# Kernel optimization log

Measured on AMD Instinct MI355X. Metric: run time of the kernel, lower is better.

## Reference

```python
import jax, jax.numpy as jnp
import numpy as np

N = 50000        # number of amino_acid nodes
E = 250000       # edges per relation
HID = 64         # resid_hidden_dim (per-head out dim)
H = 4            # num_heads
L = 2            # resid_num_layers
IN_DIM = 256     # input_dim (fc_dim output)
SCALE = 1.0 / np.sqrt(HID)
EPS_BN = 1e-5


def setup_inputs() -> dict:
    key = jax.random.key(0)
    ks = jax.random.split(key, 12)
    inp = {"x": jax.random.normal(ks[0], (N, HID), jnp.float32)}
    for i, nm in enumerate(("seq", "knn", "dis")):
        inp[f"src_{nm}"] = jax.random.randint(ks[1 + 2 * i], (E,), 0, N, dtype=jnp.int32)
        inp[f"dst_{nm}"] = jax.random.randint(ks[2 + 2 * i], (E,), 0, N, dtype=jnp.int32)
    s = 0.05
    inp["Wsrc"] = jax.random.normal(ks[7], (L, 3, HID, H * HID), jnp.float32) * s
    inp["Wdst"] = jax.random.normal(ks[8], (L, 3, HID, H * HID), jnp.float32) * s
    inp["Wfc"] = jax.random.normal(ks[9], (L, HID, HID), jnp.float32) * s
    inp["bfc"] = jnp.zeros((L, HID), jnp.float32)
    inp["gamma"] = jnp.ones((L, HID), jnp.float32)
    inp["beta"] = jnp.zeros((L, HID), jnp.float32)
    inp["Wdim"] = jax.random.normal(ks[10], (HID, IN_DIM), jnp.float32) * s
    inp["bdim"] = jnp.zeros((IN_DIM,), jnp.float32)
    return inp


def _gat_dot(x, Wsrc, Wdst, src, dst):
    # GATDotConv: q/k projections, scaled dot-product attention per edge,
    # edge-softmax over incoming edges per destination, sum aggregation.
    fs = (x @ Wsrc).reshape(N, H, HID)   # key/value (source) features
    fd = (x @ Wdst).reshape(N, H, HID)   # query (destination) features
    e = jnp.einsum("ehd,ehd->eh", fs[src], fd[dst]) * SCALE   # [E, H]
    m = jax.ops.segment_max(e, dst, num_segments=N)           # [N, H]
    m = jnp.where(jnp.isfinite(m), m, 0.0)                    # zero-in-degree safe
    p = jnp.exp(e - m[dst])
    denom = jax.ops.segment_sum(p, dst, num_segments=N)       # [N, H]
    alpha = p / jnp.maximum(denom[dst], 1e-9)                 # [E, H]
    return jax.ops.segment_sum(fs[src] * alpha[:, :, None], dst, num_segments=N)  # [N, H, HID]


def _batchnorm(x, gamma, beta):
    mu = jnp.mean(x, axis=0)
    var = jnp.var(x, axis=0)
    return gamma * (x - mu) * jax.lax.rsqrt(var + EPS_BN) + beta


def reference(x, src_seq, dst_seq, src_knn, dst_knn, src_dis, dst_dis,
              Wsrc, Wdst, Wfc, bfc, gamma, beta, Wdim, bdim):
    edges = ((src_seq, dst_seq), (src_knn, dst_knn), (src_dis, dst_dis))
    h = x
    for l in range(L):
        # HeteroGraphConv with aggregate='sum' over the three relations
        agg = jnp.zeros((N, H, HID), h.dtype)
        for r in range(3):
            agg = agg + _gat_dot(h, Wsrc[l, r], Wdst[l, r], edges[r][0], edges[r][1])
        h = jnp.mean(agg, axis=1)                       # mean over heads -> [N, HID]
        h = _batchnorm(jax.nn.relu(h @ Wfc[l] + bfc[l]), gamma[l], beta[l])
        # dropout omitted (identity in eval / deterministic reference)
    return h @ Wdim + bdim                              # [N, IN_DIM]
```

## Files before the change

kernel.cpp:

```cpp
#include <hip/hip_runtime.h>
#include <math.h>

#define N_NODES 50000
#define E_EDGES 250000
#define HID 64
#define HD 256
#define L_LAYERS 2
#define IN_DIM_ 256
#define ATT_SCALE 0.125f
#define LOG2E 1.44269504f
#define EPS_BN 1e-5f
#define NCHUNK 49
#define GX 782

#define PACK_REL (6 * 512 * 64)
#define PACK_FC  (2 * 64 * 64)
#define PACK_DIM (256 * 64)
#define HIST_B   2930
#define PACK_B   864
#define CVT_B    3125
#define PROJ_B   (GX * 8 * 3)

#define TS 72

typedef __attribute__((ext_vector_type(8))) short bf16x8;
typedef __attribute__((ext_vector_type(4))) float f32x4;

static __device__ __forceinline__ unsigned short f2bf(float f) {
    unsigned u = __float_as_uint(f);
    unsigned r = (u + 0x7fff + ((u >> 16) & 1)) >> 16;
    return (unsigned short)r;
}
static __device__ __forceinline__ float bf2f(unsigned u) {
    return __uint_as_float(u << 16);
}

static __device__ __forceinline__ float rowsum16(float x) {
    int t;
    t = __builtin_amdgcn_update_dpp(0, __float_as_int(x), 0xB1, 0xf, 0xf, true);
    x += __int_as_float(t);
    t = __builtin_amdgcn_update_dpp(0, __float_as_int(x), 0x4E, 0xf, 0xf, true);
    x += __int_as_float(t);
    t = __builtin_amdgcn_update_dpp(0, __float_as_int(x), 0x141, 0xf, 0xf, true);
    x += __int_as_float(t);
    t = __builtin_amdgcn_update_dpp(0, __float_as_int(x), 0x140, 0xf, 0xf, true);
    x += __int_as_float(t);
    return x;
}


__global__ __launch_bounds__(256) void scan_partial(const int* __restrict__ count,
                                                    int* __restrict__ bsum) {
    int b = blockIdx.x;
    int r = b / NCHUNK, ch = b - r * NCHUNK;
    int tid = threadIdx.x;
    int i0 = ch * 1024 + tid * 4;
    int s = 0;
    if (i0 + 3 < N_NODES) {
        int4 v = *(const int4*)(count + r * N_NODES + i0);
        s = v.x + v.y + v.z + v.w;
    } else {
        for (int j = 0; j < 4; ++j)
            if (i0 + j < N_NODES) s += count[r * N_NODES + i0 + j];
    }
    for (int o = 1; o < 64; o <<= 1) s += __shfl_xor(s, o, 64);
    __shared__ int wsum[4];
    if ((tid & 63) == 0) wsum[tid >> 6] = s;
    __syncthreads();
    if (tid == 0) bsum[b] = wsum[0] + wsum[1] + wsum[2] + wsum[3];
}

__global__ __launch_bounds__(256) void scan_mid(const int* __restrict__ bsum,
                                                int* __restrict__ bpre) {
    __shared__ int A[256], B[256];
    int tid = threadIdx.x;
    int v = (tid < 3 * NCHUNK) ? bsum[tid] : 0;
    int segStart = (tid / NCHUNK) * NCHUNK;
    A[tid] = v;
    __syncthreads();
    int* s = A; int* d = B;
    for (int o = 1; o < 256; o <<= 1) {
        int x = s[tid];
        if (tid - o >= segStart) x += s[tid - o];
        d[tid] = x;
        __syncthreads();
        int* t = s; s = d; d = t;
    }
    if (tid < 3 * NCHUNK) bpre[tid] = s[tid] - v;
}

__global__ __launch_bounds__(256) void scan_final(const int* __restrict__ count,
                                                  const int* __restrict__ bpre,
                                                  int* __restrict__ row_off,
                                                  int* __restrict__ cursor) {
    int b = blockIdx.x;
    int r = b / NCHUNK, ch = b - r * NCHUNK;
    int tid = threadIdx.x;
    int i0 = ch * 1024 + tid * 4;
    int v[4] = {0, 0, 0, 0};
    if (i0 + 3 < N_NODES) {
        int4 t = *(const int4*)(count + r * N_NODES + i0);
        v[0] = t.x; v[1] = t.y; v[2] = t.z; v[3] = t.w;
    } else {
        for (int j = 0; j < 4; ++j)
            if (i0 + j < N_NODES) v[j] = count[r * N_NODES + i0 + j];
    }
    int tsum = v[0] + v[1] + v[2] + v[3];
    __shared__ int A[256], B[256];
    A[tid] = tsum;
    __syncthreads();
    int* s = A; int* d = B;
    for (int o = 1; o < 256; o <<= 1) {
        int x = s[tid];
        if (tid >= o) x += s[tid - o];
        d[tid] = x;
        __syncthreads();
        int* t = s; s = d; d = t;
    }
    int run = bpre[b] + s[tid] - tsum;
    int* ro = row_off + r * (N_NODES + 1);
    int* cu = cursor + r * N_NODES;
    for (int j = 0; j < 4; ++j) {
        int idx = i0 + j;
        if (idx < N_NODES) { ro[idx] = run; cu[idx] = run; run += v[j]; }
    }
    if (ch == NCHUNK - 1 && tid == 255) ro[N_NODES] = E_EDGES;
}


__global__ __launch_bounds__(256) void u1_kernel(
        const int* __restrict__ d0, const int* __restrict__ d1, const int* __restrict__ d2,
        int* __restrict__ count,
        const float* __restrict__ Wsrc, const float* __restrict__ Wdst,
        const float* __restrict__ Wfc, const float* __restrict__ Wdim,
        unsigned short* __restrict__ WtRel, unsigned short* __restrict__ WtFc,
        unsigned short* __restrict__ WtDim,
        const float* __restrict__ x, unsigned short* __restrict__ xb) {
    int b = blockIdx.x;
    if (b < HIST_B) {
        int i = b * 256 + threadIdx.x;
        if (i < 3 * E_EDGES) {
            int r = i / E_EDGES;
            int e = i - r * E_EDGES;
            const int* dst = (r == 0) ? d0 : ((r == 1) ? d1 : d2);
            atomicAdd(&count[r * N_NODES + dst[e]], 1);
        }
    } else if (b < HIST_B + PACK_B) {
        int i = (b - HIST_B) * 256 + threadIdx.x;
        if (i < PACK_REL) {
            int k = i & 63;
            int n = (i >> 6) & 511;
            int lr = i >> 15;
            const float* srcm = (n < 256) ? Wsrc : Wdst;
            WtRel[i] = f2bf(srcm[((size_t)lr * 64 + k) * 256 + (n & 255)]);
        } else if (i < PACK_REL + PACK_FC) {
            int j = i - PACK_REL;
            int l = j >> 12, rem = j & 4095;
            int k = rem & 63, n = rem >> 6;
            WtFc[j] = f2bf(Wfc[(size_t)l * 4096 + k * 64 + n]);
        } else if (i < PACK_REL + PACK_FC + PACK_DIM) {
            int j = i - PACK_REL - PACK_FC;
            int k = j & 63, n = j >> 6;
            WtDim[j] = f2bf(Wdim[(size_t)k * 256 + n]);
        }
    } else {
        int i = ((b - HIST_B - PACK_B) * 256 + threadIdx.x) * 4;
        if (i < N_NODES * HID) {
            float4 v = *(const float4*)(x + i);
            uint2 o;
            o.x = (unsigned)f2bf(v.x) | ((unsigned)f2bf(v.y) << 16);
            o.y = (unsigned)f2bf(v.z) | ((unsigned)f2bf(v.w) << 16);
            *(uint2*)(xb + i) = o;
        }
    }
}


static __device__ __forceinline__ void proj_body(int bx, int by,
        const unsigned short* __restrict__ hB, const unsigned short* __restrict__ Wt,
        unsigned short* __restrict__ out, int M, unsigned short* tile) {
    int tid = threadIdx.x;
    int wave = tid >> 6, lane = tid & 63;
    int q = lane >> 4, li = lane & 15;
    int nodeLoc = (wave >> 1) * 32;
    int featLoc = (wave & 1) * 32;
    int nodeBase = bx * 64 + nodeLoc;
    int featBase = by * 64 + featLoc;

    const unsigned short* aptr[2];
    const unsigned short* bptr[2];
    #pragma unroll
    for (int t = 0; t < 2; ++t) {
        aptr[t] = Wt + (size_t)(featBase + t * 16 + li) * 64 + q * 8;
        int node = nodeBase + t * 16 + li; if (node >= M) node = M - 1;
        bptr[t] = hB + (size_t)node * 64 + q * 8;
    }
    f32x4 acc[2][2];
    #pragma unroll
    for (int a = 0; a < 2; ++a)
        #pragma unroll
        for (int bq = 0; bq < 2; ++bq)
            #pragma unroll
            for (int i = 0; i < 4; ++i) acc[a][bq][i] = 0.f;

    #pragma unroll
    for (int s = 0; s < 2; ++s) {
        bf16x8 a[2], b[2];
        #pragma unroll
        for (int t = 0; t < 2; ++t) {
            a[t] = *(const bf16x8*)(aptr[t] + s * 32);
            b[t] = *(const bf16x8*)(bptr[t] + s * 32);
        }
        #pragma unroll
        for (int ft = 0; ft < 2; ++ft)
            #pragma unroll
            for (int nt = 0; nt < 2; ++nt)
                acc[ft][nt] = __builtin_amdgcn_mfma_f32_16x16x32_bf16(a[ft], b[nt], acc[ft][nt], 0, 0, 0);
    }
    #pragma unroll
    for (int ft = 0; ft < 2; ++ft) {
        int fl = featLoc + ft * 16 + q * 4;
        #pragma unroll
        for (int nt = 0; nt < 2; ++nt) {
            int nl = nodeLoc + nt * 16 + li;
            unsigned lo = (unsigned)f2bf(acc[ft][nt][0]) | ((unsigned)f2bf(acc[ft][nt][1]) << 16);
            unsigned hi = (unsigned)f2bf(acc[ft][nt][2]) | ((unsigned)f2bf(acc[ft][nt][3]) << 16);
            uint2 pk; pk.x = lo; pk.y = hi;
            *(uint2*)(tile + nl * TS + fl) = pk;
        }
    }
    __syncthreads();
    #pragma unroll
    for (int p = 0; p < 2; ++p) {
        int idx = p * 256 + tid;
        int nl = idx >> 3, sg = idx & 7;
        int node = bx * 64 + nl;
        if (node < M) {
            uint4 v = *(const uint4*)(tile + nl * TS + sg * 8);
            *(uint4*)(out + (size_t)node * 512 + by * 64 + sg * 8) = v;
        }
    }
}


__global__ __launch_bounds__(256) void u2_kernel(
        const int* __restrict__ s0, const int* __restrict__ d0,
        const int* __restrict__ s1, const int* __restrict__ d1,
        const int* __restrict__ s2, const int* __restrict__ d2,
        int* __restrict__ cursor, int* __restrict__ csr_src,
        const unsigned short* __restrict__ xb, const unsigned short* __restrict__ WtRel0,
        unsigned short* __restrict__ p0, unsigned short* __restrict__ p1,
        unsigned short* __restrict__ p2) {
    __shared__ __align__(16) unsigned short tile[64 * TS];
    int b = blockIdx.x;
    if (b < HIST_B) {
        int i = b * 256 + threadIdx.x;
        if (i < 3 * E_EDGES) {
            int r = i / E_EDGES;
            int e = i - r * E_EDGES;
            const int* src = (r == 0) ? s0 : ((r == 1) ? s1 : s2);
            const int* dst = (r == 0) ? d0 : ((r == 1) ? d1 : d2);
            int dd = dst[e];
            int pos = atomicAdd(&cursor[r * N_NODES + dd], 1);
            csr_src[r * E_EDGES + pos] = src[e];
        }
    } else {
        int b2 = b - HIST_B;
        int px = b2 % GX;
        int rem = b2 / GX;
        int py = rem & 7;
        int pz = rem >> 3;
        unsigned short* out = (pz == 0) ? p0 : ((pz == 1) ? p1 : p2);
        proj_body(px, py, xb, WtRel0 + (size_t)pz * 512 * 64, out, N_NODES, tile);
    }
}

__global__ __launch_bounds__(256) void gemm_proj3(const unsigned short* __restrict__ hB,
                                                  const unsigned short* __restrict__ WtL,
                                                  unsigned short* __restrict__ p0,
                                                  unsigned short* __restrict__ p1,
                                                  unsigned short* __restrict__ p2,
                                                  int M) {
    __shared__ __align__(16) unsigned short tile[64 * TS];
    int r = blockIdx.z;
    unsigned short* out = (r == 0) ? p0 : ((r == 1) ? p1 : p2);
    proj_body(blockIdx.x, blockIdx.y, hB, WtL + (size_t)r * 512 * 64, out, M, tile);
}

__global__ __launch_bounds__(256) void gemm_f32out(const unsigned short* __restrict__ hB,
                                                   const unsigned short* __restrict__ Wt,
                                                   const float* __restrict__ bias,
                                                   float* __restrict__ out,
                                                   int M, int Nout, int relu) {
    int tid = threadIdx.x;
    int wave = tid >> 6, lane = tid & 63;
    int q = lane >> 4, li = lane & 15;
    int nodeBase = blockIdx.x * 64 + (wave >> 1) * 32;
    int featBase = blockIdx.y * 64 + (wave & 1) * 32;

    const unsigned short* aptr[2];
    const unsigned short* bptr[2];
    #pragma unroll
    for (int t = 0; t < 2; ++t) {
        aptr[t] = Wt + (size_t)(featBase + t * 16 + li) * 64 + q * 8;
        int node = nodeBase + t * 16 + li; if (node >= M) node = M - 1;
        bptr[t] = hB + (size_t)node * 64 + q * 8;
    }
    f32x4 acc[2][2];
    #pragma unroll
    for (int a = 0; a < 2; ++a)
        #pragma unroll
        for (int bq = 0; bq < 2; ++bq)
            #pragma unroll
            for (int i = 0; i < 4; ++i) acc[a][bq][i] = 0.f;

    #pragma unroll
    for (int s = 0; s < 2; ++s) {
        bf16x8 a[2], b[2];
        #pragma unroll
        for (int t = 0; t < 2; ++t) {
            a[t] = *(const bf16x8*)(aptr[t] + s * 32);
            b[t] = *(const bf16x8*)(bptr[t] + s * 32);
        }
        #pragma unroll
        for (int ft = 0; ft < 2; ++ft)
            #pragma unroll
            for (int nt = 0; nt < 2; ++nt)
                acc[ft][nt] = __builtin_amdgcn_mfma_f32_16x16x32_bf16(a[ft], b[nt], acc[ft][nt], 0, 0, 0);
    }
    #pragma unroll
    for (int ft = 0; ft < 2; ++ft) {
        int f0 = featBase + ft * 16 + q * 4;
        float b0 = bias[f0], b1 = bias[f0 + 1], b2 = bias[f0 + 2], b3 = bias[f0 + 3];
        #pragma unroll
        for (int nt = 0; nt < 2; ++nt) {
            int node = nodeBase + nt * 16 + li;
            if (node >= M) continue;
            float4 o;
            o.x = acc[ft][nt][0] + b0; o.y = acc[ft][nt][1] + b1;
            o.z = acc[ft][nt][2] + b2; o.w = acc[ft][nt][3] + b3;
            if (relu) {
                o.x = fmaxf(o.x, 0.f); o.y = fmaxf(o.y, 0.f);
                o.z = fmaxf(o.z, 0.f); o.w = fmaxf(o.w, 0.f);
            }
            *(float4*)(out + (size_t)node * Nout + f0) = o;
        }
    }
}


__global__ __launch_bounds__(256) void agg_fused(const int* __restrict__ row_off,
                                                 const int* __restrict__ csr_src,
                                                 const unsigned short* __restrict__ p0,
                                                 const unsigned short* __restrict__ p1,
                                                 const unsigned short* __restrict__ p2,
                                                 unsigned short* __restrict__ hm) {
    int wave = (blockIdx.x * 256 + threadIdx.x) >> 6;
    int lane = threadIdx.x & 63;
    if (wave >= N_NODES) return;
    int dst = wave;

    float t0 = 0.f, t1 = 0.f, t2 = 0.f, t3 = 0.f;

    #pragma unroll
    for (int r = 0; r < 3; ++r) {
        const unsigned short* proj = (r == 0) ? p0 : ((r == 1) ? p1 : p2);
        const int* ro = row_off + r * (N_NODES + 1);
        int base = ro[dst];
        int deg = ro[dst + 1] - base;
        if (deg == 0) continue;

        uint2 fdr = *(const uint2*)(proj + (size_t)dst * 512 + 256 + lane * 4);
        const float FS = ATT_SCALE * LOG2E;
        float fd0 = bf2f(fdr.x & 0xffff) * FS;
        float fd1 = __uint_as_float(fdr.x & 0xffff0000u) * FS;
        float fd2 = bf2f(fdr.y & 0xffff) * FS;
        float fd3 = __uint_as_float(fdr.y & 0xffff0000u) * FS;

        float den = 0.f;
        float a0 = 0.f, a1 = 0.f, a2 = 0.f, a3 = 0.f;
        const int* cs = csr_src + (size_t)r * E_EDGES + base;

        for (int c0 = 0; c0 < deg; c0 += 64) {
            int nc = deg - c0; if (nc > 64) nc = 64;
            int srcv = (lane < nc) ? cs[c0 + lane] : 0;
            for (int j0 = 0; j0 < nc; j0 += 16) {
                int nt = nc - j0; if (nt > 16) nt = 16;
                uint2 rowv[16];
                #pragma unroll
                for (int t = 0; t < 16; ++t) {
                    if (t < nt) {
                        int idx = __shfl(srcv, j0 + t, 64);
                        rowv[t] = *(const uint2*)(proj + (size_t)idx * 512 + lane * 4);
                    }
                }
                #pragma unroll
                for (int t = 0; t < 16; ++t) {
                    if (t < nt) {
                        float s0 = __uint_as_float(rowv[t].x << 16);
                        float s1 = __uint_as_float(rowv[t].x & 0xffff0000u);
                        float s2 = __uint_as_float(rowv[t].y << 16);
                        float s3 = __uint_as_float(rowv[t].y & 0xffff0000u);
                        float p = s0 * fd0 + s1 * fd1 + s2 * fd2 + s3 * fd3;
                        p = rowsum16(p);
                        p = fminf(fmaxf(p, -60.f), 60.f);
                        float pe = __builtin_amdgcn_exp2f(p);
                        den += pe;
                        a0 += pe * s0; a1 += pe * s1;
                        a2 += pe * s2; a3 += pe * s3;
                    }
                }
            }
        }
        float inv = 1.0f / fmaxf(den, 1e-9f);
        t0 += a0 * inv; t1 += a1 * inv; t2 += a2 * inv; t3 += a3 * inv;
    }

    t0 += __shfl_xor(t0, 16, 64); t0 += __shfl_xor(t0, 32, 64);
    t1 += __shfl_xor(t1, 16, 64); t1 += __shfl_xor(t1, 32, 64);
    t2 += __shfl_xor(t2, 16, 64); t2 += __shfl_xor(t2, 32, 64);
    t3 += __shfl_xor(t3, 16, 64); t3 += __shfl_xor(t3, 32, 64);
    if (lane < 16) {
        unsigned lo = (unsigned)f2bf(t0 * 0.25f) | ((unsigned)f2bf(t1 * 0.25f) << 16);
        unsigned hi = (unsigned)f2bf(t2 * 0.25f) | ((unsigned)f2bf(t3 * 0.25f) << 16);
        uint2 pk; pk.x = lo; pk.y = hi;
        *(uint2*)(hm + (size_t)dst * 64 + lane * 4) = pk;
    }
}


__global__ __launch_bounds__(256) void bn_reduce_kernel(const float* __restrict__ y,
                                                        float* __restrict__ acc1,
                                                        float* __restrict__ acc2) {
    int tid = threadIdx.x;
    int c = tid & 63;
    int g = tid >> 6;
    int rowStart = blockIdx.x * 4 + g;
    int stride = gridDim.x * 4;
    float s1 = 0.f, s2 = 0.f;
    for (int r = rowStart; r < N_NODES; r += stride) {
        float v = y[(size_t)r * 64 + c];
        s1 += v; s2 += v * v;
    }
    __shared__ float l1[4][64], l2[4][64];
    l1[g][c] = s1; l2[g][c] = s2;
    __syncthreads();
    if (g == 0) {
        s1 = l1[0][c] + l1[1][c] + l1[2][c] + l1[3][c];
        s2 = l2[0][c] + l2[1][c] + l2[2][c] + l2[3][c];
        atomicAdd(&acc1[c], s1);
        atomicAdd(&acc2[c], s2);
    }
}

__global__ void bn_apply_kernel(const float* __restrict__ y, const float* __restrict__ acc1,
                                const float* __restrict__ acc2, const float* __restrict__ gamma,
                                const float* __restrict__ beta,
                                unsigned short* __restrict__ outb) {
    int i = blockIdx.x * blockDim.x + threadIdx.x;
    if (i >= N_NODES * HID) return;
    int c = i & 63;
    const float invN = 1.0f / (float)N_NODES;
    float mu = acc1[c] * invN;
    float var = acc2[c] * invN - mu * mu;
    float v = gamma[c] * (y[i] - mu) * rsqrtf(var + EPS_BN) + beta[c];
    outb[i] = f2bf(v);
}


extern "C" void kernel_launch(void* const* d_in, const int* in_sizes, int n_in,
                              void* d_out, int out_size, void* d_ws, size_t ws_size,
                              hipStream_t stream) {
    const float* x     = (const float*)d_in[0];
    const int* srcs[3] = {(const int*)d_in[1], (const int*)d_in[3], (const int*)d_in[5]};
    const int* dsts[3] = {(const int*)d_in[2], (const int*)d_in[4], (const int*)d_in[6]};
    const float* Wsrc  = (const float*)d_in[7];
    const float* Wdst  = (const float*)d_in[8];
    const float* Wfc   = (const float*)d_in[9];
    const float* bfc   = (const float*)d_in[10];
    const float* gamma = (const float*)d_in[11];
    const float* beta  = (const float*)d_in[12];
    const float* Wdim  = (const float*)d_in[13];
    const float* bdim  = (const float*)d_in[14];
    float* out = (float*)d_out;

    char* ws = (char*)d_ws;
    size_t off = 0;
    auto alloc = [&](size_t bytes) -> void* {
        void* p = ws + off;
        off += (bytes + 255) & ~(size_t)255;
        return p;
    };
    float* bnacc  = (float*)alloc(256 * 4);
    int* count    = (int*)alloc((size_t)3 * N_NODES * 4);
    int* cursor   = (int*)alloc((size_t)3 * N_NODES * 4);
    int* row_off  = (int*)alloc((size_t)3 * (N_NODES + 1) * 4);
    int* csr_src  = (int*)alloc((size_t)3 * E_EDGES * 4);
    int* bsum     = (int*)alloc(256 * 4);
    int* bpre     = (int*)alloc(256 * 4);
    unsigned short* proj0 = (unsigned short*)alloc((size_t)N_NODES * 512 * 2);
    unsigned short* proj1 = (unsigned short*)alloc((size_t)N_NODES * 512 * 2);
    unsigned short* proj2 = (unsigned short*)alloc((size_t)N_NODES * 512 * 2);
    unsigned short* hm    = (unsigned short*)alloc((size_t)N_NODES * HID * 2);
    float* ybuf           = (float*)alloc((size_t)N_NODES * HID * 4);
    unsigned short* xb    = (unsigned short*)alloc((size_t)N_NODES * HID * 2);
    unsigned short* hb0   = (unsigned short*)alloc((size_t)N_NODES * HID * 2);
    unsigned short* hb1   = (unsigned short*)alloc((size_t)N_NODES * HID * 2);
    unsigned short* WtRel = (unsigned short*)alloc((size_t)PACK_REL * 2);
    unsigned short* WtFc  = (unsigned short*)alloc((size_t)PACK_FC * 2);
    unsigned short* WtDim = (unsigned short*)alloc((size_t)PACK_DIM * 2);

    hipMemsetAsync(bnacc, 0, 1024 + (size_t)3 * N_NODES * 4, stream);

    u1_kernel<<<HIST_B + PACK_B + CVT_B, 256, 0, stream>>>(
        dsts[0], dsts[1], dsts[2], count, Wsrc, Wdst, Wfc, Wdim,
        WtRel, WtFc, WtDim, x, xb);

    scan_partial<<<3 * NCHUNK, 256, 0, stream>>>(count, bsum);
    scan_mid<<<1, 256, 0, stream>>>(bsum, bpre);
    scan_final<<<3 * NCHUNK, 256, 0, stream>>>(count, bpre, row_off, cursor);

    u2_kernel<<<HIST_B + PROJ_B, 256, 0, stream>>>(
        srcs[0], dsts[0], srcs[1], dsts[1], srcs[2], dsts[2],
        cursor, csr_src, xb, WtRel, proj0, proj1, proj2);

    unsigned short* hbufs[2] = {hb0, hb1};
    const unsigned short* hcur = xb;
    for (int l = 0; l < L_LAYERS; ++l) {
        if (l > 0) {
            dim3 g(GX, 8, 3);
            gemm_proj3<<<g, 256, 0, stream>>>(hcur, WtRel + (size_t)l * 3 * 512 * 64,
                                              proj0, proj1, proj2, N_NODES);
        }
        agg_fused<<<(N_NODES + 3) / 4, 256, 0, stream>>>(row_off, csr_src,
                                                         proj0, proj1, proj2, hm);
        dim3 g2(GX, 1);
        gemm_f32out<<<g2, 256, 0, stream>>>(hm, WtFc + (size_t)l * 64 * 64, bfc + (size_t)l * HID,
                                            ybuf, N_NODES, 64, 1);
        float* ba = bnacc + l * 128;
        bn_reduce_kernel<<<256, 256, 0, stream>>>(ybuf, ba, ba + 64);
        bn_apply_kernel<<<(N_NODES * HID + 255) / 256, 256, 0, stream>>>(
            ybuf, ba, ba + 64, gamma + (size_t)l * HID, beta + (size_t)l * HID, hbufs[l]);
        hcur = hbufs[l];
    }
    dim3 g3(GX, IN_DIM_ / 64);
    gemm_f32out<<<g3, 256, 0, stream>>>(hcur, WtDim, bdim, out, N_NODES, IN_DIM_, 0);
}
```

Baseline: 590.6 us.

## Two-pass bucketed CSR build and privatized degree histogram

```diff
diff --git a/kernel.cpp b/kernel.cpp
--- a/kernel.cpp
+++ b/kernel.cpp
@@ -21,6 +21,9 @@
 #define CVT_B    3125
 #define PROJ_B   (GX * 8 * 3)
 
+#define NBUCK 391
+#define P2_B  (3 * NBUCK)
+
 #define TS 72
 
 typedef __attribute__((ext_vector_type(8))) short bf16x8;
@@ -57,11 +60,16 @@
     int i0 = ch * 1024 + tid * 4;
     int s = 0;
     if (i0 + 3 < N_NODES) {
-        int4 v = *(const int4*)(count + r * N_NODES + i0);
-        s = v.x + v.y + v.z + v.w;
+        #pragma unroll
+        for (int c = 0; c < 8; ++c) {
+            int4 v = *(const int4*)(count + (size_t)(c * 3 + r) * N_NODES + i0);
+            s += v.x + v.y + v.z + v.w;
+        }
     } else {
         for (int j = 0; j < 4; ++j)
-            if (i0 + j < N_NODES) s += count[r * N_NODES + i0 + j];
+            if (i0 + j < N_NODES)
+                for (int c = 0; c < 8; ++c)
+                    s += count[(size_t)(c * 3 + r) * N_NODES + i0 + j];
     }
     for (int o = 1; o < 64; o <<= 1) s += __shfl_xor(s, o, 64);
     __shared__ int wsum[4];
@@ -92,18 +100,24 @@
 __global__ __launch_bounds__(256) void scan_final(const int* __restrict__ count,
                                                   const int* __restrict__ bpre,
                                                   int* __restrict__ row_off,
-                                                  int* __restrict__ cursor) {
+                                                  int* __restrict__ cursor,
+                                                  int* __restrict__ bcur) {
     int b = blockIdx.x;
     int r = b / NCHUNK, ch = b - r * NCHUNK;
     int tid = threadIdx.x;
     int i0 = ch * 1024 + tid * 4;
     int v[4] = {0, 0, 0, 0};
     if (i0 + 3 < N_NODES) {
-        int4 t = *(const int4*)(count + r * N_NODES + i0);
-        v[0] = t.x; v[1] = t.y; v[2] = t.z; v[3] = t.w;
+        #pragma unroll
+        for (int c = 0; c < 8; ++c) {
+            int4 t = *(const int4*)(count + (size_t)(c * 3 + r) * N_NODES + i0);
+            v[0] += t.x; v[1] += t.y; v[2] += t.z; v[3] += t.w;
+        }
     } else {
         for (int j = 0; j < 4; ++j)
-            if (i0 + j < N_NODES) v[j] = count[r * N_NODES + i0 + j];
+            if (i0 + j < N_NODES)
+                for (int c = 0; c < 8; ++c)
+                    v[j] += count[(size_t)(c * 3 + r) * N_NODES + i0 + j];
     }
     int tsum = v[0] + v[1] + v[2] + v[3];
     __shared__ int A[256], B[256];
@@ -122,7 +136,11 @@
     int* cu = cursor + r * N_NODES;
     for (int j = 0; j < 4; ++j) {
         int idx = i0 + j;
-        if (idx < N_NODES) { ro[idx] = run; cu[idx] = run; run += v[j]; }
+        if (idx < N_NODES) {
+            ro[idx] = run; cu[idx] = run;
+            if ((idx & 127) == 0) bcur[r * NBUCK + (idx >> 7)] = run;
+            run += v[j];
+        }
     }
     if (ch == NCHUNK - 1 && tid == 255) ro[N_NODES] = E_EDGES;
 }
@@ -143,7 +161,8 @@
             int r = i / E_EDGES;
             int e = i - r * E_EDGES;
             const int* dst = (r == 0) ? d0 : ((r == 1) ? d1 : d2);
-            atomicAdd(&count[r * N_NODES + dst[e]], 1);
+            int c = b & 7;
+            atomicAdd(&count[(size_t)(c * 3 + r) * N_NODES + dst[e]], 1);
         }
     } else if (b < HIST_B + PACK_B) {
         int i = (b - HIST_B) * 256 + threadIdx.x;
@@ -176,6 +195,23 @@
 }
 
 
+__global__ __launch_bounds__(256) void eb_kernel(
+        const int* __restrict__ s0, const int* __restrict__ d0,
+        const int* __restrict__ s1, const int* __restrict__ d1,
+        const int* __restrict__ s2, const int* __restrict__ d2,
+        int* __restrict__ bcur, unsigned* __restrict__ ebuf) {
+    int i = blockIdx.x * 256 + threadIdx.x;
+    if (i >= 3 * E_EDGES) return;
+    int r = i / E_EDGES;
+    int e = i - r * E_EDGES;
+    const int* src = (r == 0) ? s0 : ((r == 1) ? s1 : s2);
+    const int* dst = (r == 0) ? d0 : ((r == 1) ? d1 : d2);
+    int d = dst[e], s = src[e];
+    int pos = atomicAdd(&bcur[r * NBUCK + (d >> 7)], 1);
+    ebuf[(size_t)r * E_EDGES + pos] = (unsigned)d | ((unsigned)s << 16);
+}
+
+
 static __device__ __forceinline__ void proj_body(int bx, int by,
         const unsigned short* __restrict__ hB, const unsigned short* __restrict__ Wt,
         unsigned short* __restrict__ out, int M, unsigned short* tile) {
@@ -243,29 +279,32 @@
 }
 
 
-__global__ __launch_bounds__(256) void u2_kernel(
-        const int* __restrict__ s0, const int* __restrict__ d0,
-        const int* __restrict__ s1, const int* __restrict__ d1,
-        const int* __restrict__ s2, const int* __restrict__ d2,
-        int* __restrict__ cursor, int* __restrict__ csr_src,
+__global__ __launch_bounds__(256) void u2b_kernel(
+        const int* __restrict__ row_off, int* __restrict__ cursor,
+        const unsigned* __restrict__ ebuf, int* __restrict__ csr_src,
         const unsigned short* __restrict__ xb, const unsigned short* __restrict__ WtRel0,
         unsigned short* __restrict__ p0, unsigned short* __restrict__ p1,
         unsigned short* __restrict__ p2) {
     __shared__ __align__(16) unsigned short tile[64 * TS];
     int b = blockIdx.x;
-    if (b < HIST_B) {
-        int i = b * 256 + threadIdx.x;
-        if (i < 3 * E_EDGES) {
-            int r = i / E_EDGES;
-            int e = i - r * E_EDGES;
-            const int* src = (r == 0) ? s0 : ((r == 1) ? s1 : s2);
-            const int* dst = (r == 0) ? d0 : ((r == 1) ? d1 : d2);
-            int dd = dst[e];
-            int pos = atomicAdd(&cursor[r * N_NODES + dd], 1);
-            csr_src[r * E_EDGES + pos] = src[e];
+    if (b < P2_B) {
+        int r = b / NBUCK, bk = b - r * NBUCK;
+        int n0 = bk << 7;
+        int n1 = n0 + 128; if (n1 > N_NODES) n1 = N_NODES;
+        const int* ro = row_off + r * (N_NODES + 1);
+        int lo = ro[n0], hi = ro[n1];
+        int* cu = cursor + r * N_NODES;
+        int* cs = csr_src + r * E_EDGES;
+        const unsigned* eb = ebuf + (size_t)r * E_EDGES;
+        for (int t = lo + threadIdx.x; t < hi; t += 256) {
+            unsigned v = eb[t];
+            int d = v & 0xffff;
+            int s = (int)(v >> 16);
+            int pos = atomicAdd(&cu[d], 1);
+            cs[pos] = s;
         }
     } else {
-        int b2 = b - HIST_B;
+        int b2 = b - P2_B;
         int px = b2 % GX;
         int rem = b2 / GX;
         int py = rem & 7;
@@ -492,10 +531,12 @@
         return p;
     };
     float* bnacc  = (float*)alloc(256 * 4);
-    int* count    = (int*)alloc((size_t)3 * N_NODES * 4);
+    int* count    = (int*)alloc((size_t)8 * 3 * N_NODES * 4);
     int* cursor   = (int*)alloc((size_t)3 * N_NODES * 4);
     int* row_off  = (int*)alloc((size_t)3 * (N_NODES + 1) * 4);
     int* csr_src  = (int*)alloc((size_t)3 * E_EDGES * 4);
+    int* bcur     = (int*)alloc((size_t)3 * NBUCK * 4);
+    unsigned* ebuf = (unsigned*)alloc((size_t)3 * E_EDGES * 4);
     int* bsum     = (int*)alloc(256 * 4);
     int* bpre     = (int*)alloc(256 * 4);
     unsigned short* proj0 = (unsigned short*)alloc((size_t)N_NODES * 512 * 2);
@@ -510,7 +551,7 @@
     unsigned short* WtFc  = (unsigned short*)alloc((size_t)PACK_FC * 2);
     unsigned short* WtDim = (unsigned short*)alloc((size_t)PACK_DIM * 2);
 
-    hipMemsetAsync(bnacc, 0, 1024 + (size_t)3 * N_NODES * 4, stream);
+    hipMemsetAsync(bnacc, 0, 1024 + (size_t)8 * 3 * N_NODES * 4, stream);
 
     u1_kernel<<<HIST_B + PACK_B + CVT_B, 256, 0, stream>>>(
         dsts[0], dsts[1], dsts[2], count, Wsrc, Wdst, Wfc, Wdim,
@@ -518,11 +559,13 @@
 
     scan_partial<<<3 * NCHUNK, 256, 0, stream>>>(count, bsum);
     scan_mid<<<1, 256, 0, stream>>>(bsum, bpre);
-    scan_final<<<3 * NCHUNK, 256, 0, stream>>>(count, bpre, row_off, cursor);
-
-    u2_kernel<<<HIST_B + PROJ_B, 256, 0, stream>>>(
-        srcs[0], dsts[0], srcs[1], dsts[1], srcs[2], dsts[2],
-        cursor, csr_src, xb, WtRel, proj0, proj1, proj2);
+    scan_final<<<3 * NCHUNK, 256, 0, stream>>>(count, bpre, row_off, cursor, bcur);
+
+    eb_kernel<<<HIST_B, 256, 0, stream>>>(
+        srcs[0], dsts[0], srcs[1], dsts[1], srcs[2], dsts[2], bcur, ebuf);
+
+    u2b_kernel<<<P2_B + PROJ_B, 256, 0, stream>>>(
+        row_off, cursor, ebuf, csr_src, xb, WtRel, proj0, proj1, proj2);
 
     unsigned short* hbufs[2] = {hb0, hb1};
     const unsigned short* hcur = xb;
```

Result: slower. 756.2 us (+28.0%).
